# Performance work log

Hardware: AMD Instinct MI355X
Metric: run time of the kernel (lower is better)

Reference implementation:

```python
import jax, jax.numpy as jnp
import numpy as np

B, M, N, C, D, H, TOPK = 32, 20000, 500000, 128, 128, 4, 100
EPS = 1e-5


def setup_inputs() -> dict:
    key = jax.random.key(0)
    ks = jax.random.split(key, 24)
    f = lambda k, s: jax.random.normal(k, s, dtype=jnp.float32) * 0.05
    inp = {
        'lhs_embedding': f(ks[0], (B, C)),
        'rhs_gnn_embedding': f(ks[1], (M, C)),
        'rhs_emb_weight': f(ks[2], (N, D)),
        'proj_W': f(ks[3], (D, C)), 'proj_b': jnp.zeros((D,), jnp.float32),
        'head_W': f(ks[4], (1, C)), 'head_b': jnp.zeros((1,), jnp.float32),
        'off_emb_W': f(ks[5], (1, D)), 'off_emb_b': jnp.zeros((1,), jnp.float32),
        'off_id_W': f(ks[6], (1, D)), 'off_id_b': jnp.zeros((1,), jnp.float32),
        'Wq': f(ks[7], (D, D)), 'bq': jnp.zeros((D,), jnp.float32),
        'Wk': f(ks[8], (D, D)), 'bk': jnp.zeros((D,), jnp.float32),
        'Wv': f(ks[9], (D, D)), 'bv': jnp.zeros((D,), jnp.float32),
        'Wo': f(ks[10], (D, D)), 'bo': jnp.zeros((D,), jnp.float32),
        'ln1_g': jnp.ones((D,), jnp.float32), 'ln1_b': jnp.zeros((D,), jnp.float32),
        'ffn_W': f(ks[11], (D, D)), 'ffn_b': jnp.zeros((D,), jnp.float32),
        'ln2_g': jnp.ones((D,), jnp.float32), 'ln2_b': jnp.zeros((D,), jnp.float32),
        'rhs_idgnn_index': jax.random.randint(ks[12], (M,), 0, N, dtype=jnp.int32),
        'lhs_idgnn_batch': jnp.sort(jax.random.randint(ks[13], (M,), 0, B, dtype=jnp.int32)),
    }
    return inp


def _ln(x, g, b):
    mu = jnp.mean(x, axis=-1, keepdims=True)
    var = jnp.mean(jnp.square(x - mu), axis=-1, keepdims=True)
    return (x - mu) * jax.lax.rsqrt(var + EPS) * g + b


def reference(lhs_embedding, rhs_gnn_embedding, rhs_emb_weight, proj_W, proj_b,
              head_W, head_b, off_emb_W, off_emb_b, off_id_W, off_id_b,
              Wq, bq, Wk, bk, Wv, bv, Wo, bo, ln1_g, ln1_b, ffn_W, ffn_b,
              ln2_g, ln2_b, rhs_idgnn_index, lhs_idgnn_batch):
    # --- embgnn logits: dense [B,N] matmul + per-row offset ---
    lhs_proj = lhs_embedding @ proj_W.T + proj_b                          # [B,D]
    embgnn_logits = lhs_proj @ rhs_emb_weight.T                           # [B,N]
    embgnn_logits = embgnn_logits + (lhs_proj @ off_emb_W[0] + off_emb_b[0])[:, None]

    # --- idgnn logits on sampled rhs nodes ---
    idgnn_logits = rhs_gnn_embedding @ head_W[0] + head_b[0]              # [M]
    idgnn_logits = idgnn_logits + jnp.sum(lhs_embedding[lhs_idgnn_batch] * rhs_gnn_embedding, axis=-1)
    idgnn_offset = lhs_proj @ off_id_W[0] + off_id_b[0]                   # [B]
    idgnn_logits = idgnn_logits + idgnn_offset[lhs_idgnn_batch]

    # scatter idgnn logits into the dense logits tensor
    embgnn_logits = embgnn_logits.at[lhs_idgnn_batch, rhs_idgnn_index].set(idgnn_logits)

    # --- final rhs embeddings: shallow table + scattered GNN embeddings ---
    copy_tensor = jnp.zeros_like(rhs_emb_weight).at[rhs_idgnn_index].set(rhs_gnn_embedding)
    final_rhs_embed = rhs_emb_weight + copy_tensor                        # [N,D]

    # --- rerank: topk -> gather -> MAB -> scatter back ---
    _, topk_index = jax.lax.top_k(embgnn_logits, TOPK)                    # [B,TOPK]
    top_embed = final_rhs_embed[topk_index]                               # [B,TOPK,D]

    dh = D // H
    q = (top_embed @ Wq.T + bq).reshape(B, TOPK, H, dh)
    k = (top_embed @ Wk.T + bk).reshape(B, TOPK, H, dh)
    v = (top_embed @ Wv.T + bv).reshape(B, TOPK, H, dh)
    att = jnp.einsum('bthd,bshd->bhts', q, k) / jnp.sqrt(jnp.float32(dh))
    att = jax.nn.softmax(att, axis=-1)
    o = jnp.einsum('bhts,bshd->bthd', att, v).reshape(B, TOPK, D) @ Wo.T + bo
    x = _ln(top_embed + o, ln1_g, ln1_b)
    x = _ln(x + jax.nn.relu(x @ ffn_W.T + ffn_b), ln2_g, ln2_b)           # tr_embed [B,TOPK,D]

    # original code passes lhs_proj[lhs_idgnn_batch] and indexes rows 0..B-1
    lhs_q = lhs_proj[lhs_idgnn_batch][:B]                                 # [B,D]
    scores = jnp.sum(lhs_q[:, None, :] * x, axis=-1)                      # [B,TOPK]
    rows = jnp.arange(B)[:, None]
    transformer_logits = jnp.full((B, N), -jnp.inf, dtype=embgnn_logits.dtype)
    transformer_logits = transformer_logits.at[rows, topk_index].set(scores)

    return embgnn_logits, transformer_logits, topk_index
```

## Files before the change

### kernel.cpp

```cpp
#include <hip/hip_runtime.h>

typedef unsigned long long u64;
typedef unsigned int u32;

#define N_NODES 500000
#define M_SAMP  20000
#define BB      32
#define DD      128
#define TOPK    100
#define NBINS   2048
#define CAP     2048
#define C4PB    3907
#define LN_EPS  1e-5f
#define NEG_BIG -1.0e30f

__device__ __forceinline__ u32 fkey(float x) {
  u32 u = __float_as_uint(x);
  u32 mask = (u32)((int)u >> 31) | 0x80000000u;
  return u ^ mask;
}

__global__ __launch_bounds__(256) void k_front(
    const float* __restrict__ lhs, const float* __restrict__ pW,
    const float* __restrict__ pb, const float* __restrict__ oeW,
    const float* __restrict__ oeb, const float* __restrict__ oiW,
    const float* __restrict__ oib, const float* __restrict__ rgnn,
    const float* __restrict__ hW, const float* __restrict__ hb,
    const int* __restrict__ ridx, const int* __restrict__ rbat,
    float* __restrict__ lhs_proj, float* __restrict__ lhs_projT,
    float* __restrict__ oe_sc, float* __restrict__ oi_sc,
    float* __restrict__ val, int* __restrict__ win,
    int* __restrict__ inv, u32* __restrict__ hist) {
  int bid = blockIdx.x, tid = threadIdx.x;
  if (bid < 32) {
    __shared__ float lrow[DD];
    __shared__ float red[DD];
    int b = bid, d = tid;
    if (d < DD) lrow[d] = lhs[b * DD + d];
    __syncthreads();
    float acc = 0.f;
    if (d < DD) {
      acc = pb[d];
      for (int c = 0; c < DD; ++c) acc += lrow[c] * pW[d * DD + c];
      lhs_proj[b * DD + d] = acc;
      lhs_projT[d * BB + b] = acc;
      red[d] = acc * oeW[d];
    }
    __syncthreads();
    for (int s = 64; s > 0; s >>= 1) { if (d < s) red[d] += red[d + s]; __syncthreads(); }
    if (d == 0) oe_sc[b] = red[0] + oeb[0];
    __syncthreads();
    if (d < DD) red[d] = acc * oiW[d];
    __syncthreads();
    for (int s = 64; s > 0; s >>= 1) { if (d < s) red[d] += red[d + s]; __syncthreads(); }
    if (d == 0) oi_sc[b] = red[0] + oib[0];
  } else if (bid < 32 + M_SAMP / 4) {
    int wid = tid >> 6, lane = tid & 63;
    int m = (bid - 32) * 4 + wid;
    if (m >= M_SAMP) return;
    int b = rbat[m], n = ridx[m];
    float2 rg = ((const float2*)(rgnn + (size_t)m * DD))[lane];
    float2 hw = ((const float2*)hW)[lane];
    float2 le = ((const float2*)(lhs + (size_t)b * DD))[lane];
    float p = rg.x * hw.x + rg.y * hw.y + rg.x * le.x + rg.y * le.y;
    for (int off = 32; off > 0; off >>= 1) p += __shfl_down(p, off);
    int w = 1;
    for (int j0 = m + 1; j0 < M_SAMP; j0 += 64) {
      int j = j0 + lane;
      bool inb = (j < M_SAMP) && (rbat[j] == b);
      bool match = inb && (ridx[j] == n);
      if (__ballot(match)) { w = 0; break; }
      if (__ballot(inb) != ~0ULL) break;
    }
    if (lane == 0) { val[m] = p + hb[0]; win[m] = w; }
  } else {
    int i = (bid - (32 + M_SAMP / 4)) * 256 + tid;
    if (i < N_NODES) inv[i] = -1;
    if (i < BB * NBINS) hist[i] = 0;
  }
}

__global__ __launch_bounds__(256) void k_embgnn(const float* __restrict__ rhs,
    const float* __restrict__ lhsT, const float* __restrict__ oe_sc,
    float* __restrict__ out, float* __restrict__ tr) {
  __shared__ float sT[64][DD + 4];
  int tid = threadIdx.x;
  long n0 = (long)blockIdx.x * 64;
  #pragma unroll
  for (int p = 0; p < 8; ++p) {
    int f = p * 256 + tid;
    int r = f >> 5, c4 = (f & 31) << 2;
    long n = n0 + r; if (n >= N_NODES) n = N_NODES - 1;
    float4 v = *(const float4*)(rhs + n * DD + c4);
    sT[r][c4] = v.x; sT[r][c4 + 1] = v.y; sT[r][c4 + 2] = v.z; sT[r][c4 + 3] = v.w;
  }
  __syncthreads();
  int lane = tid & 63;
  int bg = __builtin_amdgcn_readfirstlane((tid >> 6) * 8);
  float acc[8];
  #pragma unroll
  for (int j = 0; j < 8; ++j) acc[j] = 0.f;
  const float4* srow = (const float4*)&sT[lane][0];
  #pragma unroll 4
  for (int cq = 0; cq < 32; ++cq) {
    float4 rv = srow[cq];
    const float* lp = lhsT + cq * 4 * BB + bg;
    #pragma unroll
    for (int j = 0; j < 8; ++j) {
      acc[j] += lp[j] * rv.x;
      acc[j] += lp[BB + j] * rv.y;
      acc[j] += lp[2 * BB + j] * rv.z;
      acc[j] += lp[3 * BB + j] * rv.w;
    }
  }
  long n = n0 + lane;
  if (n < N_NODES) {
    #pragma unroll
    for (int j = 0; j < 8; ++j) {
      out[(long)(bg + j) * N_NODES + n] = acc[j] + oe_sc[bg + j];
      tr[(long)(bg + j) * N_NODES + n] = NEG_BIG;
    }
  }
}

__global__ void k_scatter2(const int* __restrict__ ridx, const int* __restrict__ rbat,
                           const float* __restrict__ val, const int* __restrict__ win,
                           const float* __restrict__ oi_sc,
                           int* __restrict__ inv, float* __restrict__ out) {
  int m = blockIdx.x * 256 + threadIdx.x;
  if (m < M_SAMP) {
    atomicMax(&inv[ridx[m]], m);
    if (win[m]) {
      int b = rbat[m];
      out[(long)b * N_NODES + ridx[m]] = val[m] + oi_sc[b];
    }
  }
}

__global__ void k_hist(const float* __restrict__ out, u32* __restrict__ hist) {
  __shared__ u32 hsh[NBINS];
  int tid = threadIdx.x;
  for (int i = tid; i < NBINS; i += 256) hsh[i] = 0;
  __syncthreads();
  int row = blockIdx.y;
  const float4* o4 = (const float4*)out + (long)row * (N_NODES / 4);
  int start = blockIdx.x * C4PB;
  int end = min(start + C4PB, N_NODES / 4);
  for (int i = start + tid; i < end; i += 256) {
    float4 v = o4[i];
    atomicAdd(&hsh[fkey(v.x) >> 21], 1u);
    atomicAdd(&hsh[fkey(v.y) >> 21], 1u);
    atomicAdd(&hsh[fkey(v.z) >> 21], 1u);
    atomicAdd(&hsh[fkey(v.w) >> 21], 1u);
  }
  __syncthreads();
  for (int i = tid; i < NBINS; i += 256)
    if (hsh[i]) atomicAdd(&hist[row * NBINS + i], hsh[i]);
}

__global__ __launch_bounds__(1024) void k_topk(const float* __restrict__ out,
                                               const u32* __restrict__ hist,
                                               int* __restrict__ topk_out) {
  __shared__ u64 sh[CAP];
  __shared__ u32 part[256];
  __shared__ int s_cb;
  __shared__ u32 s_cnt;
  int tid = threadIdx.x, row = blockIdx.x;
  const u32* hrow = hist + row * NBINS;
  if (tid < 256) {
    u32 p = 0;
    #pragma unroll
    for (int j = 0; j < 8; ++j) p += hrow[tid * 8 + j];
    part[tid] = p;
  }
  if (tid == 0) s_cnt = 0;
  __syncthreads();
  if (tid == 0) {
    u32 cum = 0; int g = 255, found = 0;
    for (; g > 0; --g) { cum += part[g]; if (cum >= TOPK) { found = 1; break; } }
    u32 c2 = found ? (cum - part[g]) : cum;
    int hi = found ? g * 8 + 7 : 7;
    int bin;
    for (bin = hi; bin > 0; --bin) { c2 += hrow[bin]; if (c2 >= TOPK) break; }
    s_cb = bin;
  }
  __syncthreads();
  u32 cb = (u32)s_cb;
  const float4* o4 = (const float4*)out + (long)row * (N_NODES / 4);
  for (int i = tid; i < N_NODES / 4; i += 1024) {
    float4 v = o4[i];
    u32 kk[4] = { fkey(v.x), fkey(v.y), fkey(v.z), fkey(v.w) };
    #pragma unroll
    for (int j = 0; j < 4; ++j) {
      if ((kk[j] >> 21) >= cb) {
        u32 pos = atomicAdd(&s_cnt, 1u);
        int idx = i * 4 + j;
        if (pos < CAP) sh[pos] = ((u64)kk[j] << 32) | (u32)(~idx);
      }
    }
  }
  __syncthreads();
  int cnt = min((int)s_cnt, CAP);
  int NS = 128; while (NS < cnt) NS <<= 1;
  for (int i = cnt + tid; i < NS; i += 1024) sh[i] = 0ULL;
  __syncthreads();
  for (int k2 = 2; k2 <= NS; k2 <<= 1) {
    for (int j = k2 >> 1; j > 0; j >>= 1) {
      for (int i = tid; i < NS; i += 1024) {
        int ixj = i ^ j;
        if (ixj > i) {
          u64 a = sh[i], c = sh[ixj];
          bool up = ((i & k2) == 0);
          if (up ? (a < c) : (a > c)) { sh[i] = c; sh[ixj] = a; }
        }
      }
      __syncthreads();
    }
  }
  if (tid < TOPK) topk_out[row * TOPK + tid] = (int)(~(u32)sh[tid]);
}

__global__ __launch_bounds__(128) void k_gqkv(const int* __restrict__ topk,
    const int* __restrict__ inv, const float* __restrict__ rhs_emb,
    const float* __restrict__ rgnn,
    const float* __restrict__ Wq, const float* __restrict__ bq,
    const float* __restrict__ Wk, const float* __restrict__ bk,
    const float* __restrict__ Wv, const float* __restrict__ bv,
    float* __restrict__ q, float* __restrict__ k_, float* __restrict__ v_) {
  __shared__ float xr[16][DD];
  __shared__ int sn[16], sm[16];
  int tid = threadIdx.x;
  long r0 = (long)blockIdx.x * 16;
  if (tid < 16) { int n = topk[r0 + tid]; sn[tid] = n; sm[tid] = inv[n]; }
  __syncthreads();
  for (int i = tid; i < 16 * DD; i += 128) {
    int r = i >> 7, dd_ = i & 127;
    int n = sn[r], mw = sm[r];
    float v = rhs_emb[(long)n * DD + dd_];
    if (mw >= 0) v += rgnn[(long)mw * DD + dd_];
    xr[r][dd_] = v;
  }
  __syncthreads();
  float aq[16], ak[16], av[16];
  float bqv = bq[tid], bkv = bk[tid], bvv = bv[tid];
  #pragma unroll
  for (int r = 0; r < 16; ++r) { aq[r] = bqv; ak[r] = bkv; av[r] = bvv; }
  const float4* Wq4 = (const float4*)(Wq + tid * DD);
  const float4* Wk4 = (const float4*)(Wk + tid * DD);
  const float4* Wv4 = (const float4*)(Wv + tid * DD);
  #pragma unroll 4
  for (int c4 = 0; c4 < 32; ++c4) {
    float4 wq = Wq4[c4], wk = Wk4[c4], wv = Wv4[c4];
    #pragma unroll
    for (int r = 0; r < 16; ++r) {
      const float* xa = &xr[r][c4 << 2];
      float x0v = xa[0], x1v = xa[1], x2v = xa[2], x3v = xa[3];
      aq[r] += x0v * wq.x + x1v * wq.y + x2v * wq.z + x3v * wq.w;
      ak[r] += x0v * wk.x + x1v * wk.y + x2v * wk.z + x3v * wk.w;
      av[r] += x0v * wv.x + x1v * wv.y + x2v * wv.z + x3v * wv.w;
    }
  }
  #pragma unroll
  for (int r = 0; r < 16; ++r) {
    q[(r0 + r) * DD + tid] = aq[r];
    k_[(r0 + r) * DD + tid] = ak[r];
    v_[(r0 + r) * DD + tid] = av[r];
  }
}

__global__ __launch_bounds__(128) void k_att(const float* __restrict__ q,
    const float* __restrict__ k_, const float* __restrict__ v_, float* __restrict__ o) {
  __shared__ float kv[TOPK][32];
  __shared__ float att[TOPK][TOPK];
  int b = blockIdx.x >> 2, h = blockIdx.x & 3;
  int tid = threadIdx.x;
  long base = (long)b * TOPK * DD + h * 32;
  for (int i = tid; i < TOPK * 32; i += 128) {
    int t = i >> 5, d = i & 31;
    kv[t][d] = k_[base + (long)t * DD + d];
  }
  __syncthreads();
  int t = tid;
  if (t < TOPK) {
    float4 q4[8];
    const float4* qp = (const float4*)(q + base + (long)t * DD);
    #pragma unroll
    for (int i = 0; i < 8; ++i) q4[i] = qp[i];
    float qreg[32];
    #pragma unroll
    for (int i = 0; i < 8; ++i) {
      qreg[4 * i] = q4[i].x; qreg[4 * i + 1] = q4[i].y;
      qreg[4 * i + 2] = q4[i].z; qreg[4 * i + 3] = q4[i].w;
    }
    const float scale = 0.17677669529663687f;
    for (int s = 0; s < TOPK; ++s) {
      float sum = 0.f;
      #pragma unroll
      for (int d = 0; d < 32; ++d) sum += qreg[d] * kv[s][d];
      att[t][s] = sum * scale;
    }
    float mx = att[t][0];
    for (int s = 1; s < TOPK; ++s) mx = fmaxf(mx, att[t][s]);
    float sum = 0.f;
    for (int s = 0; s < TOPK; ++s) { float e = expf(att[t][s] - mx); att[t][s] = e; sum += e; }
    float inv = 1.f / sum;
    for (int s = 0; s < TOPK; ++s) att[t][s] *= inv;
  }
  __syncthreads();
  for (int i = tid; i < TOPK * 32; i += 128) {
    int tt = i >> 5, d = i & 31;
    kv[tt][d] = v_[base + (long)tt * DD + d];
  }
  __syncthreads();
  if (t < TOPK) {
    float osum[32];
    #pragma unroll
    for (int d = 0; d < 32; ++d) osum[d] = 0.f;
    for (int s = 0; s < TOPK; ++s) {
      float a = att[t][s];
      #pragma unroll
      for (int d = 0; d < 32; ++d) osum[d] += a * kv[s][d];
    }
    float4* op = (float4*)(o + base + (long)t * DD);
    #pragma unroll
    for (int i = 0; i < 8; ++i)
      op[i] = make_float4(osum[4 * i], osum[4 * i + 1], osum[4 * i + 2], osum[4 * i + 3]);
  }
}

__global__ __launch_bounds__(128) void k_xform(const float* __restrict__ ob_,
    const float* __restrict__ Wo, const float* __restrict__ bo,
    const int* __restrict__ topk, const int* __restrict__ inv,
    const float* __restrict__ rhs_emb, const float* __restrict__ rgnn,
    const float* __restrict__ g1, const float* __restrict__ be1,
    const float* __restrict__ fW, const float* __restrict__ fb,
    const float* __restrict__ g2, const float* __restrict__ be2,
    const float* __restrict__ lhs_proj, const int* __restrict__ lbat,
    float* __restrict__ tr) {
  __shared__ float sA[16][DD];
  __shared__ float sT[16][DD + 4];
  __shared__ float sMu[16], sRs[16];
  __shared__ int sn[16], sm[16];
  int tid = threadIdx.x;
  long r0 = (long)blockIdx.x * 16;
  if (tid < 16) { int n = topk[r0 + tid]; sn[tid] = n; sm[tid] = inv[n]; }
  for (int i = tid; i < 16 * DD; i += 128) sA[i >> 7][i & 127] = ob_[r0 * DD + i];
  __syncthreads();
  float vacc[16];
  #pragma unroll
  for (int r = 0; r < 16; ++r) vacc[r] = bo[tid];
  const float4* Wo4 = (const float4*)(Wo + tid * DD);
  #pragma unroll 4
  for (int c4 = 0; c4 < 32; ++c4) {
    float4 w = Wo4[c4];
    #pragma unroll
    for (int r = 0; r < 16; ++r) {
      const float* xa = &sA[r][c4 << 2];
      vacc[r] += xa[0] * w.x + xa[1] * w.y + xa[2] * w.z + xa[3] * w.w;
    }
  }
  float tval[16];
  #pragma unroll
  for (int r = 0; r < 16; ++r) {
    float x0v = rhs_emb[(long)sn[r] * DD + tid];
    if (sm[r] >= 0) x0v += rgnn[(long)sm[r] * DD + tid];
    tval[r] = vacc[r] + x0v;
    sT[r][tid] = tval[r];
  }
  __syncthreads();
  int rr = tid >> 3, sub = tid & 7;
  {
    float s = 0.f, qq = 0.f;
    const float* tp = &sT[rr][sub * 16];
    #pragma unroll
    for (int j = 0; j < 16; ++j) { float v = tp[j]; s += v; qq += v * v; }
    s += __shfl_xor(s, 1); qq += __shfl_xor(qq, 1);
    s += __shfl_xor(s, 2); qq += __shfl_xor(qq, 2);
    s += __shfl_xor(s, 4); qq += __shfl_xor(qq, 4);
    if (sub == 0) {
      float mu = s * (1.f / 128.f);
      sMu[rr] = mu;
      sRs[rr] = rsqrtf(fmaxf(qq * (1.f / 128.f) - mu * mu, 0.f) + LN_EPS);
    }
  }
  __syncthreads();
  float g1v = g1[tid], b1v = be1[tid];
  float x1v[16];
  #pragma unroll
  for (int r = 0; r < 16; ++r) {
    x1v[r] = (tval[r] - sMu[r]) * sRs[r] * g1v + b1v;
    sA[r][tid] = x1v[r];
  }
  __syncthreads();
  #pragma unroll
  for (int r = 0; r < 16; ++r) vacc[r] = fb[tid];
  const float4* fW4 = (const float4*)(fW + tid * DD);
  #pragma unroll 4
  for (int c4 = 0; c4 < 32; ++c4) {
    float4 w = fW4[c4];
    #pragma unroll
    for (int r = 0; r < 16; ++r) {
      const float* xa = &sA[r][c4 << 2];
      vacc[r] += xa[0] * w.x + xa[1] * w.y + xa[2] * w.z + xa[3] * w.w;
    }
  }
  float t2[16];
  #pragma unroll
  for (int r = 0; r < 16; ++r) { t2[r] = x1v[r] + fmaxf(vacc[r], 0.f); sT[r][tid] = t2[r]; }
  __syncthreads();
  {
    float s = 0.f, qq = 0.f;
    const float* tp = &sT[rr][sub * 16];
    #pragma unroll
    for (int j = 0; j < 16; ++j) { float v = tp[j]; s += v; qq += v * v; }
    s += __shfl_xor(s, 1); qq += __shfl_xor(qq, 1);
    s += __shfl_xor(s, 2); qq += __shfl_xor(qq, 2);
    s += __shfl_xor(s, 4); qq += __shfl_xor(qq, 4);
    if (sub == 0) {
      float mu = s * (1.f / 128.f);
      sMu[rr] = mu;
      sRs[rr] = rsqrtf(fmaxf(qq * (1.f / 128.f) - mu * mu, 0.f) + LN_EPS);
    }
  }
  __syncthreads();
  float g2v = g2[tid], b2v = be2[tid];
  #pragma unroll
  for (int r = 0; r < 16; ++r) {
    long row = r0 + r;
    int b = (int)(row / TOPK);
    float lq = lhs_proj[(long)lbat[b] * DD + tid];
    float x2 = (t2[r] - sMu[r]) * sRs[r] * g2v + b2v;
    sT[r][tid] = x2 * lq;
  }
  __syncthreads();
  {
    float s = 0.f;
    const float* tp = &sT[rr][sub * 16];
    #pragma unroll
    for (int j = 0; j < 16; ++j) s += tp[j];
    s += __shfl_xor(s, 1);
    s += __shfl_xor(s, 2);
    s += __shfl_xor(s, 4);
    if (sub == 0) {
      long row = r0 + rr;
      int b = (int)(row / TOPK);
      tr[(long)b * N_NODES + topk[row]] = s;
    }
  }
}

extern "C" void kernel_launch(void* const* d_in, const int* in_sizes, int n_in,
                              void* d_out, int out_size, void* d_ws, size_t ws_size,
                              hipStream_t stream) {
  const float* lhs_emb  = (const float*)d_in[0];
  const float* rgnn     = (const float*)d_in[1];
  const float* rhs_emb  = (const float*)d_in[2];
  const float* proj_W   = (const float*)d_in[3];
  const float* proj_b   = (const float*)d_in[4];
  const float* head_W   = (const float*)d_in[5];
  const float* head_b   = (const float*)d_in[6];
  const float* off_emb_W= (const float*)d_in[7];
  const float* off_emb_b= (const float*)d_in[8];
  const float* off_id_W = (const float*)d_in[9];
  const float* off_id_b = (const float*)d_in[10];
  const float* Wq = (const float*)d_in[11]; const float* bq = (const float*)d_in[12];
  const float* Wk = (const float*)d_in[13]; const float* bk = (const float*)d_in[14];
  const float* Wv = (const float*)d_in[15]; const float* bv = (const float*)d_in[16];
  const float* Wo = (const float*)d_in[17]; const float* bo = (const float*)d_in[18];
  const float* ln1_g = (const float*)d_in[19]; const float* ln1_b = (const float*)d_in[20];
  const float* ffn_W = (const float*)d_in[21]; const float* ffn_b = (const float*)d_in[22];
  const float* ln2_g = (const float*)d_in[23]; const float* ln2_b = (const float*)d_in[24];
  const int* ridx = (const int*)d_in[25];
  const int* rbat = (const int*)d_in[26];

  float* out_emb = (float*)d_out;
  float* out_tr  = out_emb + (long)BB * N_NODES;
  int*   out_topk = (int*)(out_emb + 2L * BB * N_NODES);

  char* w = (char*)d_ws;
  float* lhs_proj  = (float*)w; w += 16384;
  float* lhs_projT = (float*)w; w += 16384;
  float* oe_sc    = (float*)w; w += 128;
  float* oi_sc    = (float*)w; w += 128;
  float* idval    = (float*)w; w += 80000;
  int*   idwin    = (int*)w;   w += 80000;
  int*   inv      = (int*)w;   w += 2000000;
  u32*   hist     = (u32*)w;   w += BB * NBINS * 4;
  float* qb = (float*)w; w += 1638400;
  float* kb = (float*)w; w += 1638400;
  float* vb = (float*)w; w += 1638400;
  float* ob = (float*)w; w += 1638400;

  const int SETUP_BLKS = (N_NODES + 255) / 256;
  k_front<<<32 + M_SAMP / 4 + SETUP_BLKS, 256, 0, stream>>>(
      lhs_emb, proj_W, proj_b, off_emb_W, off_emb_b, off_id_W, off_id_b,
      rgnn, head_W, head_b, ridx, rbat,
      lhs_proj, lhs_projT, oe_sc, oi_sc, idval, idwin, inv, hist);
  k_embgnn<<<(N_NODES + 63) / 64, 256, 0, stream>>>(rhs_emb, lhs_projT, oe_sc,
                                                    out_emb, out_tr);
  k_scatter2<<<(M_SAMP + 255) / 256, 256, 0, stream>>>(ridx, rbat, idval, idwin,
                                                       oi_sc, inv, out_emb);
  k_hist<<<dim3(32, BB), 256, 0, stream>>>(out_emb, hist);
  k_topk<<<BB, 1024, 0, stream>>>(out_emb, hist, out_topk);

  k_gqkv<<<BB * TOPK / 16, 128, 0, stream>>>(out_topk, inv, rhs_emb, rgnn,
                                             Wq, bq, Wk, bk, Wv, bv, qb, kb, vb);
  k_att<<<BB * 4, 128, 0, stream>>>(qb, kb, vb, ob);
  k_xform<<<BB * TOPK / 16, 128, 0, stream>>>(ob, Wo, bo, out_topk, inv,
                                              rhs_emb, rgnn, ln1_g, ln1_b,
                                              ffn_W, ffn_b, ln2_g, ln2_b,
                                              lhs_proj, rbat, out_tr);
}
```

Measured before the change: 312.1 us.

## Split top-k into parallel candidate collection and per-row sort kernels

The single-block-per-row top-k kernel that scanned all 500k logits and then bitonic-sorted them is split into two kernels. A grid of 32x32 blocks applies the histogram threshold and appends candidates to a global buffer through global atomics, and a second per-row kernel loads those candidates and sorts them. The aim is to spread the 64MB candidate scan over many more CUs instead of only 32 blocks. The cost is an extra launch, global atomic contention on the per-row counters, and a workspace round trip for candidates.

```diff
diff --git a/kernel.cpp b/kernel.cpp
--- a/kernel.cpp
+++ b/kernel.cpp
@@ -30,7 +30,7 @@
     float* __restrict__ lhs_proj, float* __restrict__ lhs_projT,
     float* __restrict__ oe_sc, float* __restrict__ oi_sc,
     float* __restrict__ val, int* __restrict__ win,
-    int* __restrict__ inv, u32* __restrict__ hist) {
+    int* __restrict__ inv, u32* __restrict__ hist, u32* __restrict__ cand_cnt) {
   int bid = blockIdx.x, tid = threadIdx.x;
   if (bid < 32) {
     __shared__ float lrow[DD];
@@ -77,6 +77,7 @@
     int i = (bid - (32 + M_SAMP / 4)) * 256 + tid;
     if (i < N_NODES) inv[i] = -1;
     if (i < BB * NBINS) hist[i] = 0;
+    if (i < BB) cand_cnt[i] = 0;
   }
 }
 
@@ -158,22 +159,16 @@
     if (hsh[i]) atomicAdd(&hist[row * NBINS + i], hsh[i]);
 }
 
-__global__ __launch_bounds__(1024) void k_topk(const float* __restrict__ out,
-                                               const u32* __restrict__ hist,
-                                               int* __restrict__ topk_out) {
-  __shared__ u64 sh[CAP];
+__global__ void k_collect(const float* __restrict__ out, const u32* __restrict__ hist,
+                          u32* __restrict__ cand_cnt, u64* __restrict__ cand) {
   __shared__ u32 part[256];
   __shared__ int s_cb;
-  __shared__ u32 s_cnt;
-  int tid = threadIdx.x, row = blockIdx.x;
+  int tid = threadIdx.x, row = blockIdx.y;
   const u32* hrow = hist + row * NBINS;
-  if (tid < 256) {
-    u32 p = 0;
-    #pragma unroll
-    for (int j = 0; j < 8; ++j) p += hrow[tid * 8 + j];
-    part[tid] = p;
-  }
-  if (tid == 0) s_cnt = 0;
+  u32 p = 0;
+  #pragma unroll
+  for (int j = 0; j < 8; ++j) p += hrow[tid * 8 + j];
+  part[tid] = p;
   __syncthreads();
   if (tid == 0) {
     u32 cum = 0; int g = 255, found = 0;
@@ -187,22 +182,30 @@
   __syncthreads();
   u32 cb = (u32)s_cb;
   const float4* o4 = (const float4*)out + (long)row * (N_NODES / 4);
-  for (int i = tid; i < N_NODES / 4; i += 1024) {
+  int start = blockIdx.x * C4PB;
+  int end = min(start + C4PB, N_NODES / 4);
+  for (int i = start + tid; i < end; i += 256) {
     float4 v = o4[i];
     u32 kk[4] = { fkey(v.x), fkey(v.y), fkey(v.z), fkey(v.w) };
     #pragma unroll
     for (int j = 0; j < 4; ++j) {
       if ((kk[j] >> 21) >= cb) {
-        u32 pos = atomicAdd(&s_cnt, 1u);
+        u32 pos = atomicAdd(&cand_cnt[row], 1u);
         int idx = i * 4 + j;
-        if (pos < CAP) sh[pos] = ((u64)kk[j] << 32) | (u32)(~idx);
+        if (pos < CAP) cand[(long)row * CAP + pos] = ((u64)kk[j] << 32) | (u32)(~idx);
       }
     }
   }
-  __syncthreads();
-  int cnt = min((int)s_cnt, CAP);
+}
+
+__global__ __launch_bounds__(1024) void k_sort(const u64* __restrict__ cand,
+                                               const u32* __restrict__ cand_cnt,
+                                               int* __restrict__ topk_out) {
+  __shared__ u64 sh[CAP];
+  int row = blockIdx.x, tid = threadIdx.x;
+  int cnt = min((int)cand_cnt[row], CAP);
   int NS = 128; while (NS < cnt) NS <<= 1;
-  for (int i = cnt + tid; i < NS; i += 1024) sh[i] = 0ULL;
+  for (int i = tid; i < NS; i += 1024) sh[i] = (i < cnt) ? cand[(long)row * CAP + i] : 0ULL;
   __syncthreads();
   for (int k2 = 2; k2 <= NS; k2 <<= 1) {
     for (int j = k2 >> 1; j > 0; j >>= 1) {
@@ -486,6 +489,8 @@
   int*   idwin    = (int*)w;   w += 80000;
   int*   inv      = (int*)w;   w += 2000000;
   u32*   hist     = (u32*)w;   w += BB * NBINS * 4;
+  u32*   cand_cnt = (u32*)w;   w += 128;
+  u64*   cand     = (u64*)w;   w += (long)BB * CAP * 8;
   float* qb = (float*)w; w += 1638400;
   float* kb = (float*)w; w += 1638400;
   float* vb = (float*)w; w += 1638400;
@@ -495,13 +500,14 @@
   k_front<<<32 + M_SAMP / 4 + SETUP_BLKS, 256, 0, stream>>>(
       lhs_emb, proj_W, proj_b, off_emb_W, off_emb_b, off_id_W, off_id_b,
       rgnn, head_W, head_b, ridx, rbat,
-      lhs_proj, lhs_projT, oe_sc, oi_sc, idval, idwin, inv, hist);
+      lhs_proj, lhs_projT, oe_sc, oi_sc, idval, idwin, inv, hist, cand_cnt);
   k_embgnn<<<(N_NODES + 63) / 64, 256, 0, stream>>>(rhs_emb, lhs_projT, oe_sc,
                                                     out_emb, out_tr);
   k_scatter2<<<(M_SAMP + 255) / 256, 256, 0, stream>>>(ridx, rbat, idval, idwin,
                                                        oi_sc, inv, out_emb);
   k_hist<<<dim3(32, BB), 256, 0, stream>>>(out_emb, hist);
-  k_topk<<<BB, 1024, 0, stream>>>(out_emb, hist, out_topk);
+  k_collect<<<dim3(32, BB), 256, 0, stream>>>(out_emb, hist, cand_cnt, cand);
+  k_sort<<<BB, 1024, 0, stream>>>(cand, cand_cnt, out_topk);
 
   k_gqkv<<<BB * TOPK / 16, 128, 0, stream>>>(out_topk, inv, rhs_emb, rgnn,
                                              Wq, bq, Wk, bk, Wv, bv, qb, kb, vb);
```

New measurement: 322.3 us. +3.3%, slower.

## Fuse scatter and histogram into a per-row top-k kernel, drop global hist

Applied to the files above, without the earlier changes.

Removes the separate scatter and histogram kernels. The atomicMax inverse-index build moves into the first blocks of the embgnn kernel. The per-row idgnn scatter, the histogram (now held in shared memory with 4-way replicated bins to cut atomic contention) and the top-k selection all run inside one 1024-thread block per batch row. This saves two launches and the global histogram zeroing and atomics. In exchange, the histogram pass now runs on only 32 blocks, so it has far less parallelism than the previous 32x32 grid and must read each 2 MB row twice from a single block.

```diff
diff --git a/kernel.cpp b/kernel.cpp
--- a/kernel.cpp
+++ b/kernel.cpp
@@ -29,8 +29,7 @@
     const int* __restrict__ ridx, const int* __restrict__ rbat,
     float* __restrict__ lhs_proj, float* __restrict__ lhs_projT,
     float* __restrict__ oe_sc, float* __restrict__ oi_sc,
-    float* __restrict__ val, int* __restrict__ win,
-    int* __restrict__ inv, u32* __restrict__ hist) {
+    float* __restrict__ val, int* __restrict__ win, int* __restrict__ inv) {
   int bid = blockIdx.x, tid = threadIdx.x;
   if (bid < 32) {
     __shared__ float lrow[DD];
@@ -76,15 +75,19 @@
   } else {
     int i = (bid - (32 + M_SAMP / 4)) * 256 + tid;
     if (i < N_NODES) inv[i] = -1;
-    if (i < BB * NBINS) hist[i] = 0;
   }
 }
 
 __global__ __launch_bounds__(256) void k_embgnn(const float* __restrict__ rhs,
     const float* __restrict__ lhsT, const float* __restrict__ oe_sc,
+    const int* __restrict__ ridx, int* __restrict__ inv,
     float* __restrict__ out, float* __restrict__ tr) {
   __shared__ float sT[64][DD + 4];
   int tid = threadIdx.x;
+  if (blockIdx.x < (M_SAMP + 255) / 256) {
+    int m = blockIdx.x * 256 + tid;
+    if (m < M_SAMP) atomicMax(&inv[ridx[m]], m);
+  }
   long n0 = (long)blockIdx.x * 64;
   #pragma unroll
   for (int p = 0; p < 8; ++p) {
@@ -123,57 +126,53 @@
   }
 }
 
-__global__ void k_scatter2(const int* __restrict__ ridx, const int* __restrict__ rbat,
-                           const float* __restrict__ val, const int* __restrict__ win,
-                           const float* __restrict__ oi_sc,
-                           int* __restrict__ inv, float* __restrict__ out) {
-  int m = blockIdx.x * 256 + threadIdx.x;
-  if (m < M_SAMP) {
-    atomicMax(&inv[ridx[m]], m);
-    if (win[m]) {
-      int b = rbat[m];
-      out[(long)b * N_NODES + ridx[m]] = val[m] + oi_sc[b];
-    }
-  }
-}
-
-__global__ void k_hist(const float* __restrict__ out, u32* __restrict__ hist) {
-  __shared__ u32 hsh[NBINS];
-  int tid = threadIdx.x;
-  for (int i = tid; i < NBINS; i += 256) hsh[i] = 0;
-  __syncthreads();
-  int row = blockIdx.y;
-  const float4* o4 = (const float4*)out + (long)row * (N_NODES / 4);
-  int start = blockIdx.x * C4PB;
-  int end = min(start + C4PB, N_NODES / 4);
-  for (int i = start + tid; i < end; i += 256) {
-    float4 v = o4[i];
-    atomicAdd(&hsh[fkey(v.x) >> 21], 1u);
-    atomicAdd(&hsh[fkey(v.y) >> 21], 1u);
-    atomicAdd(&hsh[fkey(v.z) >> 21], 1u);
-    atomicAdd(&hsh[fkey(v.w) >> 21], 1u);
-  }
-  __syncthreads();
-  for (int i = tid; i < NBINS; i += 256)
-    if (hsh[i]) atomicAdd(&hist[row * NBINS + i], hsh[i]);
-}
-
-__global__ __launch_bounds__(1024) void k_topk(const float* __restrict__ out,
-                                               const u32* __restrict__ hist,
-                                               int* __restrict__ topk_out) {
+__global__ __launch_bounds__(1024) void k_topk32(float* out,
+    const int* __restrict__ ridx, const int* __restrict__ rbat,
+    const float* __restrict__ val, const int* __restrict__ win,
+    const float* __restrict__ oi_sc, int* __restrict__ topk_out) {
+  __shared__ u32 hsh[NBINS * 4];
   __shared__ u64 sh[CAP];
   __shared__ u32 part[256];
-  __shared__ int s_cb;
+  __shared__ int s_lo, s_hi, s_cb;
   __shared__ u32 s_cnt;
-  int tid = threadIdx.x, row = blockIdx.x;
-  const u32* hrow = hist + row * NBINS;
+  int tid = threadIdx.x, b = blockIdx.x;
+  long rowbase = (long)b * N_NODES;
+  #pragma unroll
+  for (int i = 0; i < 8; ++i) hsh[tid + i * 1024] = 0;
+  if (tid == 0) {
+    s_cnt = 0;
+    int l = 0, r = M_SAMP;
+    while (l < r) { int mid = (l + r) >> 1; if (rbat[mid] < b) l = mid + 1; else r = mid; }
+    s_lo = l;
+    r = M_SAMP;
+    while (l < r) { int mid = (l + r) >> 1; if (rbat[mid] <= b) l = mid + 1; else r = mid; }
+    s_hi = l;
+  }
+  __syncthreads();
+  float oib = oi_sc[b];
+  for (int m = s_lo + tid; m < s_hi; m += 1024)
+    if (win[m]) out[rowbase + ridx[m]] = val[m] + oib;
+  __threadfence();
+  __syncthreads();
+  const float4* o4 = (const float4*)(out + rowbase);
+  int rep = tid & 3;
+  for (int i = tid; i < N_NODES / 4; i += 1024) {
+    float4 v = o4[i];
+    atomicAdd(&hsh[(fkey(v.x) >> 21) * 4 + rep], 1u);
+    atomicAdd(&hsh[(fkey(v.y) >> 21) * 4 + rep], 1u);
+    atomicAdd(&hsh[(fkey(v.z) >> 21) * 4 + rep], 1u);
+    atomicAdd(&hsh[(fkey(v.w) >> 21) * 4 + rep], 1u);
+  }
+  __syncthreads();
   if (tid < 256) {
     u32 p = 0;
     #pragma unroll
-    for (int j = 0; j < 8; ++j) p += hrow[tid * 8 + j];
+    for (int j = 0; j < 8; ++j) {
+      int bin = tid * 8 + j;
+      p += hsh[bin * 4] + hsh[bin * 4 + 1] + hsh[bin * 4 + 2] + hsh[bin * 4 + 3];
+    }
     part[tid] = p;
   }
-  if (tid == 0) s_cnt = 0;
   __syncthreads();
   if (tid == 0) {
     u32 cum = 0; int g = 255, found = 0;
@@ -181,12 +180,14 @@
     u32 c2 = found ? (cum - part[g]) : cum;
     int hi = found ? g * 8 + 7 : 7;
     int bin;
-    for (bin = hi; bin > 0; --bin) { c2 += hrow[bin]; if (c2 >= TOPK) break; }
+    for (bin = hi; bin > 0; --bin) {
+      c2 += hsh[bin * 4] + hsh[bin * 4 + 1] + hsh[bin * 4 + 2] + hsh[bin * 4 + 3];
+      if (c2 >= TOPK) break;
+    }
     s_cb = bin;
   }
   __syncthreads();
   u32 cb = (u32)s_cb;
-  const float4* o4 = (const float4*)out + (long)row * (N_NODES / 4);
   for (int i = tid; i < N_NODES / 4; i += 1024) {
     float4 v = o4[i];
     u32 kk[4] = { fkey(v.x), fkey(v.y), fkey(v.z), fkey(v.w) };
@@ -194,8 +195,7 @@
     for (int j = 0; j < 4; ++j) {
       if ((kk[j] >> 21) >= cb) {
         u32 pos = atomicAdd(&s_cnt, 1u);
-        int idx = i * 4 + j;
-        if (pos < CAP) sh[pos] = ((u64)kk[j] << 32) | (u32)(~idx);
+        if (pos < CAP) sh[pos] = ((u64)kk[j] << 32) | (u32)(~(i * 4 + j));
       }
     }
   }
@@ -217,7 +217,7 @@
       __syncthreads();
     }
   }
-  if (tid < TOPK) topk_out[row * TOPK + tid] = (int)(~(u32)sh[tid]);
+  if (tid < TOPK) topk_out[b * TOPK + tid] = (int)(~(u32)sh[tid]);
 }
 
 __global__ __launch_bounds__(128) void k_gqkv(const int* __restrict__ topk,
@@ -485,7 +485,6 @@
   float* idval    = (float*)w; w += 80000;
   int*   idwin    = (int*)w;   w += 80000;
   int*   inv      = (int*)w;   w += 2000000;
-  u32*   hist     = (u32*)w;   w += BB * NBINS * 4;
   float* qb = (float*)w; w += 1638400;
   float* kb = (float*)w; w += 1638400;
   float* vb = (float*)w; w += 1638400;
@@ -495,14 +494,11 @@
   k_front<<<32 + M_SAMP / 4 + SETUP_BLKS, 256, 0, stream>>>(
       lhs_emb, proj_W, proj_b, off_emb_W, off_emb_b, off_id_W, off_id_b,
       rgnn, head_W, head_b, ridx, rbat,
-      lhs_proj, lhs_projT, oe_sc, oi_sc, idval, idwin, inv, hist);
+      lhs_proj, lhs_projT, oe_sc, oi_sc, idval, idwin, inv);
   k_embgnn<<<(N_NODES + 63) / 64, 256, 0, stream>>>(rhs_emb, lhs_projT, oe_sc,
-                                                    out_emb, out_tr);
-  k_scatter2<<<(M_SAMP + 255) / 256, 256, 0, stream>>>(ridx, rbat, idval, idwin,
-                                                       oi_sc, inv, out_emb);
-  k_hist<<<dim3(32, BB), 256, 0, stream>>>(out_emb, hist);
-  k_topk<<<BB, 1024, 0, stream>>>(out_emb, hist, out_topk);
-
+                                                    ridx, inv, out_emb, out_tr);
+  k_topk32<<<BB, 1024, 0, stream>>>(out_emb, ridx, rbat, idval, idwin, oi_sc,
+                                    out_topk);
   k_gqkv<<<BB * TOPK / 16, 128, 0, stream>>>(out_topk, inv, rhs_emb, rgnn,
                                              Wq, bq, Wk, bk, Wv, bv, qb, kb, vb);
   k_att<<<BB * 4, 128, 0, stream>>>(qb, kb, vb, ob);
```

New measurement: 351.9 us. 1.13x slower.

## Fold idgnn scatter into histogram kernel and inverse-index into embgnn

Applied to the files above, without the earlier changes.

Removes the separate scatter kernel. The inverse-index atomicMax moves into the first blocks of the embgnn kernel, and the per-row idgnn overwrite moves into the histogram kernel, which uses a binary search over the sorted batch array to find each row's sample range before histogramming its chunk. The shared histogram is replicated twice to reduce atomic contention, and the histogram zeroing moves to a memset. This saves one launch and one pass over the sample arrays. In exchange, each histogram block does a serial binary search and scans all samples for its row, and ordering now relies on the overwrite happening before the block reads its own chunk.

```diff
diff --git a/kernel.cpp b/kernel.cpp
--- a/kernel.cpp
+++ b/kernel.cpp
@@ -29,8 +29,7 @@
     const int* __restrict__ ridx, const int* __restrict__ rbat,
     float* __restrict__ lhs_proj, float* __restrict__ lhs_projT,
     float* __restrict__ oe_sc, float* __restrict__ oi_sc,
-    float* __restrict__ val, int* __restrict__ win,
-    int* __restrict__ inv, u32* __restrict__ hist) {
+    float* __restrict__ val, int* __restrict__ win, int* __restrict__ inv) {
   int bid = blockIdx.x, tid = threadIdx.x;
   if (bid < 32) {
     __shared__ float lrow[DD];
@@ -76,15 +75,19 @@
   } else {
     int i = (bid - (32 + M_SAMP / 4)) * 256 + tid;
     if (i < N_NODES) inv[i] = -1;
-    if (i < BB * NBINS) hist[i] = 0;
   }
 }
 
 __global__ __launch_bounds__(256) void k_embgnn(const float* __restrict__ rhs,
     const float* __restrict__ lhsT, const float* __restrict__ oe_sc,
+    const int* __restrict__ ridx, int* __restrict__ inv,
     float* __restrict__ out, float* __restrict__ tr) {
   __shared__ float sT[64][DD + 4];
   int tid = threadIdx.x;
+  if (blockIdx.x < (M_SAMP + 255) / 256) {
+    int m = blockIdx.x * 256 + tid;
+    if (m < M_SAMP) atomicMax(&inv[ridx[m]], m);
+  }
   long n0 = (long)blockIdx.x * 64;
   #pragma unroll
   for (int p = 0; p < 8; ++p) {
@@ -123,39 +126,48 @@
   }
 }
 
-__global__ void k_scatter2(const int* __restrict__ ridx, const int* __restrict__ rbat,
-                           const float* __restrict__ val, const int* __restrict__ win,
-                           const float* __restrict__ oi_sc,
-                           int* __restrict__ inv, float* __restrict__ out) {
-  int m = blockIdx.x * 256 + threadIdx.x;
-  if (m < M_SAMP) {
-    atomicMax(&inv[ridx[m]], m);
-    if (win[m]) {
-      int b = rbat[m];
-      out[(long)b * N_NODES + ridx[m]] = val[m] + oi_sc[b];
-    }
-  }
-}
-
-__global__ void k_hist(const float* __restrict__ out, u32* __restrict__ hist) {
-  __shared__ u32 hsh[NBINS];
-  int tid = threadIdx.x;
-  for (int i = tid; i < NBINS; i += 256) hsh[i] = 0;
-  __syncthreads();
-  int row = blockIdx.y;
-  const float4* o4 = (const float4*)out + (long)row * (N_NODES / 4);
+__global__ void k_hist(float* out, u32* __restrict__ hist,
+                       const int* __restrict__ ridx, const int* __restrict__ rbat,
+                       const float* __restrict__ val, const int* __restrict__ win,
+                       const float* __restrict__ oi_sc) {
+  __shared__ u32 hsh[NBINS * 2];
+  __shared__ int s_lo, s_hi;
+  int tid = threadIdx.x, row = blockIdx.y;
+  for (int i = tid; i < NBINS * 2; i += 256) hsh[i] = 0;
+  if (tid == 0) {
+    int l = 0, r = M_SAMP;
+    while (l < r) { int mid = (l + r) >> 1; if (rbat[mid] < row) l = mid + 1; else r = mid; }
+    s_lo = l;
+    r = M_SAMP;
+    while (l < r) { int mid = (l + r) >> 1; if (rbat[mid] <= row) l = mid + 1; else r = mid; }
+    s_hi = l;
+  }
+  __syncthreads();
+  long rowbase = (long)row * N_NODES;
   int start = blockIdx.x * C4PB;
   int end = min(start + C4PB, N_NODES / 4);
+  int i0 = start * 4, i1 = end * 4;
+  float oib = oi_sc[row];
+  for (int m = s_lo + tid; m < s_hi; m += 256) {
+    int ix = ridx[m];
+    if (win[m] && ix >= i0 && ix < i1) out[rowbase + ix] = val[m] + oib;
+  }
+  __threadfence_block();
+  __syncthreads();
+  const float4* o4 = (const float4*)out + rowbase / 4;
+  int rep = tid & 1;
   for (int i = start + tid; i < end; i += 256) {
     float4 v = o4[i];
-    atomicAdd(&hsh[fkey(v.x) >> 21], 1u);
-    atomicAdd(&hsh[fkey(v.y) >> 21], 1u);
-    atomicAdd(&hsh[fkey(v.z) >> 21], 1u);
-    atomicAdd(&hsh[fkey(v.w) >> 21], 1u);
-  }
-  __syncthreads();
-  for (int i = tid; i < NBINS; i += 256)
-    if (hsh[i]) atomicAdd(&hist[row * NBINS + i], hsh[i]);
+    atomicAdd(&hsh[(fkey(v.x) >> 21) * 2 + rep], 1u);
+    atomicAdd(&hsh[(fkey(v.y) >> 21) * 2 + rep], 1u);
+    atomicAdd(&hsh[(fkey(v.z) >> 21) * 2 + rep], 1u);
+    atomicAdd(&hsh[(fkey(v.w) >> 21) * 2 + rep], 1u);
+  }
+  __syncthreads();
+  for (int i = tid; i < NBINS; i += 256) {
+    u32 s = hsh[i * 2] + hsh[i * 2 + 1];
+    if (s) atomicAdd(&hist[row * NBINS + i], s);
+  }
 }
 
 __global__ __launch_bounds__(1024) void k_topk(const float* __restrict__ out,
@@ -194,8 +206,7 @@
     for (int j = 0; j < 4; ++j) {
       if ((kk[j] >> 21) >= cb) {
         u32 pos = atomicAdd(&s_cnt, 1u);
-        int idx = i * 4 + j;
-        if (pos < CAP) sh[pos] = ((u64)kk[j] << 32) | (u32)(~idx);
+        if (pos < CAP) sh[pos] = ((u64)kk[j] << 32) | (u32)(~(i * 4 + j));
       }
     }
   }
@@ -491,18 +502,18 @@
   float* vb = (float*)w; w += 1638400;
   float* ob = (float*)w; w += 1638400;
 
+  hipMemsetAsync(hist, 0, BB * NBINS * 4, stream);
+
   const int SETUP_BLKS = (N_NODES + 255) / 256;
   k_front<<<32 + M_SAMP / 4 + SETUP_BLKS, 256, 0, stream>>>(
       lhs_emb, proj_W, proj_b, off_emb_W, off_emb_b, off_id_W, off_id_b,
       rgnn, head_W, head_b, ridx, rbat,
-      lhs_proj, lhs_projT, oe_sc, oi_sc, idval, idwin, inv, hist);
+      lhs_proj, lhs_projT, oe_sc, oi_sc, idval, idwin, inv);
   k_embgnn<<<(N_NODES + 63) / 64, 256, 0, stream>>>(rhs_emb, lhs_projT, oe_sc,
-                                                    out_emb, out_tr);
-  k_scatter2<<<(M_SAMP + 255) / 256, 256, 0, stream>>>(ridx, rbat, idval, idwin,
-                                                       oi_sc, inv, out_emb);
-  k_hist<<<dim3(32, BB), 256, 0, stream>>>(out_emb, hist);
+                                                    ridx, inv, out_emb, out_tr);
+  k_hist<<<dim3(32, BB), 256, 0, stream>>>(out_emb, hist, ridx, rbat,
+                                           idval, idwin, oi_sc);
   k_topk<<<BB, 1024, 0, stream>>>(out_emb, hist, out_topk);
-
   k_gqkv<<<BB * TOPK / 16, 128, 0, stream>>>(out_topk, inv, rhs_emb, rgnn,
                                              Wq, bq, Wk, bk, Wv, bv, qb, kb, vb);
   k_att<<<BB * 4, 128, 0, stream>>>(qb, kb, vb, ob);
```

New measurement: 315.8 us. About the same (+1.2%).
